# Kernel tuning notes

Hardware: AMD Instinct MI355X
Metric: run time of the kernel (lower is better)

## Reference

```python
import jax, jax.numpy as jnp
import numpy as np

T, B, D_IN = 128, 256, 600   # timesteps, batch, encoded input dim
N_RIMS, K_ACT = 6, 4          # rims per layer, active rims (top-k)
D_HID = 600 // N_RIMS         # hidden dim per RIM = 100
D_K, D_V = 64, 400            # input-attention key/value proj dims (in_d_v = cell input dim)


def setup_inputs() -> dict:
    key = jax.random.key(0)
    ks = jax.random.split(key, 8)
    g = lambda k, shape, s: (jax.random.normal(k, shape, jnp.float32) * s)
    return {
        "x": jax.random.normal(ks[0], (T, B, D_IN), jnp.float32),
        # input attention: per-RIM query proj, shared key/value proj over encoded input
        "Wq": g(ks[1], (N_RIMS, D_HID, D_K), 0.05),
        "Wk": g(ks[2], (D_IN, D_K), 0.05),
        "Wv": g(ks[3], (D_IN, D_V), 0.05),
        # block-diagonal (per-RIM) GRU params
        "W_ih": g(ks[4], (N_RIMS, D_V, 3 * D_HID), 0.05),
        "W_hh": g(ks[5], (N_RIMS, D_HID, 3 * D_HID), 0.05),
        "b_ih": jnp.zeros((N_RIMS, 3 * D_HID), jnp.float32),
        "b_hh": jnp.zeros((N_RIMS, 3 * D_HID), jnp.float32),
    }


def reference(x, Wq, Wk, Wv, W_ih, W_hh, b_ih, b_hh):
    scale = 1.0 / jnp.sqrt(jnp.float32(D_K))

    def step(h, xt):
        # --- input attention over [real input, null row] (num_modules_read_input = 2) ---
        kx = xt @ Wk                                   # [B, D_K] key for real input (null key = 0)
        vx = xt @ Wv                                   # [B, D_V] value for real input (null value = 0)
        q = jnp.einsum('bnh,nhk->bnk', h, Wq)          # [B, N, D_K] per-RIM queries
        s_in = jnp.einsum('bnk,bk->bn', q, kx) * scale # score vs real input; null score = 0
        probs = jax.nn.softmax(jnp.stack([s_in, jnp.zeros_like(s_in)], axis=-1), axis=-1)
        p_in = probs[..., 0]                           # [B, N] attention on real input
        attn_out = p_in[..., None] * vx[:, None, :]    # [B, N, D_V] (null value is zero)
        # --- active-RIM mask: top-k rims attending most to the real input ---
        _, idx = jax.lax.top_k(p_in, K_ACT)            # [B, K]
        mask = jnp.zeros_like(p_in).at[jnp.arange(B)[:, None], idx].set(1.0)[..., None]  # [B, N, 1]
        # --- block-diagonal GRU cell (blockified params: independent per RIM) ---
        gi = jnp.einsum('bnd,ndk->bnk', attn_out, W_ih) + b_ih
        gh = jnp.einsum('bnh,nhk->bnk', h, W_hh) + b_hh
        i_r, i_z, i_n = jnp.split(gi, 3, axis=-1)
        h_r, h_z, h_n = jnp.split(gh, 3, axis=-1)
        r = jax.nn.sigmoid(i_r + h_r)
        z = jax.nn.sigmoid(i_z + h_z)
        n = jnp.tanh(i_n + r * h_n)
        h_new = (1.0 - z) * n + z * h
        # inactive rims keep their old state; output is mask * hidden
        h_next = mask * h_new + (1.0 - mask) * h
        return h_next, mask * h_new                    # [B, N, D_HID]

    h0 = jnp.zeros((B, N_RIMS, D_HID), x.dtype)
    _, out = jax.lax.scan(step, h0, x)                 # out: [T, B, N_RIMS, D_HID]
    return out
```

## Files before the change

### kernel.cpp

```cpp
#include <hip/hip_runtime.h>
#include <cstddef>

#define TSTEPS 128
#define BATCH  256
#define DIN    600
#define NR     6
#define KACT   4
#define DH     100
#define DK     64
#define DV     400
#define G3     300
#define LD1    512
#define LDG    1920

__global__ __launch_bounds__(256) void build_w1(const float* __restrict__ Wk,
                                                const float* __restrict__ Wv,
                                                float* __restrict__ W1) {
  int idx = blockIdx.x * 256 + threadIdx.x;
  if (idx >= DIN * LD1) return;
  int d = idx >> 9, c = idx & (LD1 - 1);
  float v = 0.f;
  if (c < DK)            v = Wk[d * DK + c];
  else if (c < DK + DV)  v = Wv[d * DV + (c - DK)];
  W1[idx] = v;
}

__global__ __launch_bounds__(256) void build_wt(const float* __restrict__ Wih,
                                                float* __restrict__ WT) {
  int idx = blockIdx.x * 256 + threadIdx.x;
  if (idx >= DV * LDG) return;
  int v = idx / LDG, c = idx - v * LDG;
  float w = 0.f;
  if (c < NR * G3) { int n = c / G3, j = c - n * G3; w = Wih[(n * DV + v) * G3 + j]; }
  WT[idx] = w;
}

__global__ __launch_bounds__(256) void sgemm_k(const float* __restrict__ A, int lda,
                                               const float* __restrict__ B, int ldb,
                                               float* __restrict__ C, int ldc, int K) {
  __shared__ float As[8][132];
  __shared__ float Bs[8][128];
  const int tid = threadIdx.x;
  const int tx = tid & 15, ty = tid >> 4;
  const size_t m0 = (size_t)blockIdx.x * 128, n0 = (size_t)blockIdx.y * 128;
  const int arow = tid >> 1, akq = (tid & 1) * 4;
  const int brow = tid >> 5, bcol = (tid & 31) * 4;
  const float* Ap = A + (m0 + arow) * (size_t)lda + akq;
  const float* Bp = B + (size_t)brow * ldb + n0 + bcol;

  float acc[8][8];
#pragma unroll
  for (int i = 0; i < 8; ++i)
#pragma unroll
    for (int j = 0; j < 8; ++j) acc[i][j] = 0.f;

  for (int k0 = 0; k0 < K; k0 += 8) {
    float4 av = *(const float4*)(Ap + k0);
    float4 bv = *(const float4*)(Bp + (size_t)k0 * ldb);
    __syncthreads();
    As[akq + 0][arow] = av.x;
    As[akq + 1][arow] = av.y;
    As[akq + 2][arow] = av.z;
    As[akq + 3][arow] = av.w;
    *(float4*)&Bs[brow][bcol] = bv;
    __syncthreads();
#pragma unroll
    for (int k = 0; k < 8; ++k) {
      float a[8], b[8];
#pragma unroll
      for (int i = 0; i < 8; ++i) a[i] = As[k][ty * 8 + i];
#pragma unroll
      for (int j = 0; j < 8; ++j) b[j] = Bs[k][tx * 8 + j];
#pragma unroll
      for (int i = 0; i < 8; ++i)
#pragma unroll
        for (int j = 0; j < 8; ++j) acc[i][j] += a[i] * b[j];
    }
  }

  float* Cp = C + (m0 + (size_t)ty * 8) * ldc + n0 + tx * 8;
#pragma unroll
  for (int i = 0; i < 8; ++i) {
    float4 v0 = make_float4(acc[i][0], acc[i][1], acc[i][2], acc[i][3]);
    float4 v1 = make_float4(acc[i][4], acc[i][5], acc[i][6], acc[i][7]);
    *(float4*)(Cp + (size_t)i * ldc)     = v0;
    *(float4*)(Cp + (size_t)i * ldc + 4) = v1;
  }
}

__global__ __launch_bounds__(512) void rim_scan(
    const float* __restrict__ PRE1, const float* __restrict__ GX,
    const float* __restrict__ Wq,   const float* __restrict__ Whh,
    const float* __restrict__ bih,  const float* __restrict__ bhh,
    float* __restrict__ out, float* __restrict__ hstate,
    unsigned long long* __restrict__ pbuf,
    int t0, int tc, int first) {
  __shared__ __align__(16) float wbuf[G3 * DH];
  __shared__ __align__(16) float wqbuf[DK * DH];
  __shared__ __align__(16) float hbuf[8 * DH];
  __shared__ float pl[8][NR];

  const int tid = threadIdx.x;
  const int g = blockIdx.x & 31;
  const int n = blockIdx.x >> 5;

  {
    const float* wsrc = Whh + (size_t)n * (DH * G3);
    for (int i = tid; i < DH * G3; i += 512) {
      int hh = i / G3, c = i - hh * G3;
      wbuf[c * DH + hh] = wsrc[i];
    }
    const float* qsrc = Wq + (size_t)n * (DH * DK);
    for (int i = tid; i < DH * DK; i += 512) {
      int hh = i >> 6, k = i & 63;
      wqbuf[k * DH + hh] = qsrc[i];
    }
    if (first) {
      for (int i = tid; i < 8 * DH; i += 512) hbuf[i] = 0.f;
    } else {
      for (int i = tid; i < 8 * DH; i += 512) {
        int b = i / DH, hh = i - b * DH;
        hbuf[b * DH + hh] = hstate[((size_t)(g * 8 + b) * NR + n) * DH + hh];
      }
    }
  }
  __syncthreads();

  const bool isQ = tid >= 256;
  const int ho = tid & 127;
  const bool act_t = (!isQ) && (ho < DH);
  const int half = (tid >> 7) & 1;
  const int bbase = half * 4;
  const int kq = tid & 63;
  const int bp2 = (tid >> 6) & 3;

  float bi0 = 0.f, bi1 = 0.f, bi2 = 0.f, bh0 = 0.f, bh1 = 0.f, bh2 = 0.f;
  if (act_t) {
    const float* bi = bih + (size_t)n * G3 + ho;
    const float* bh = bhh + (size_t)n * G3 + ho;
    bi0 = bi[0]; bi1 = bi[DH]; bi2 = bi[2 * DH];
    bh0 = bh[0]; bh1 = bh[DH]; bh2 = bh[2 * DH];
  }

  const float4* wr = (const float4*)&wbuf[ho * DH];
  const float4* wz = (const float4*)&wbuf[(ho + 100) * DH];
  const float4* wn = (const float4*)&wbuf[(ho + 200) * DH];
  const float4* wq4 = (const float4*)&wqbuf[kq * DH];
  const float4* h40 = (const float4*)&hbuf[(bbase + 0) * DH];
  const float4* h41 = (const float4*)&hbuf[(bbase + 1) * DH];
  const float4* h42 = (const float4*)&hbuf[(bbase + 2) * DH];
  const float4* h43 = (const float4*)&hbuf[(bbase + 3) * DH];
  const float4* hqA = (const float4*)&hbuf[bp2 * DH];
  const float4* hqB = (const float4*)&hbuf[(bp2 + 4) * DH];

  for (int tl = 0; tl < tc; ++tl) {
    const int t = t0 + tl;
    const int par = t & 1;

    float gx[4][3];
    float acc[4][3];

    if (isQ) {
      float kx0 = PRE1[((size_t)tl * BATCH + g * 8 + bp2) * LD1 + kq];
      float kx1 = PRE1[((size_t)tl * BATCH + g * 8 + bp2 + 4) * LD1 + kq];
      float a0 = 0.f, a1 = 0.f;
#pragma unroll 5
      for (int q4 = 0; q4 < 25; ++q4) {
        float4 w = wq4[q4];
        float4 v0 = hqA[q4];
        float4 v1 = hqB[q4];
        a0 += v0.x * w.x; a0 += v0.y * w.y; a0 += v0.z * w.z; a0 += v0.w * w.w;
        a1 += v1.x * w.x; a1 += v1.y * w.y; a1 += v1.z * w.z; a1 += v1.w * w.w;
      }
      float s0 = a0 * kx0, s1 = a1 * kx1;
#pragma unroll
      for (int off = 1; off < 64; off <<= 1) {
        s0 += __shfl_xor(s0, off);
        s1 += __shfl_xor(s1, off);
      }
      if (kq == 0) {
        float sa = s0 * 0.125f;
        float ma = sa > 0.f ? sa : 0.f;
        float pa = expf(sa - ma) / (expf(sa - ma) + expf(-ma));
        float sb = s1 * 0.125f;
        float mb = sb > 0.f ? sb : 0.f;
        float pb = expf(sb - mb) / (expf(sb - mb) + expf(-mb));
        unsigned long long tag = ((unsigned long long)(unsigned)(t + 1)) << 32;
        __hip_atomic_store(&pbuf[(((size_t)par * 32 + g) * NR + n) * 8 + bp2],
                           tag | __float_as_uint(pa),
                           __ATOMIC_RELAXED, __HIP_MEMORY_SCOPE_AGENT);
        __hip_atomic_store(&pbuf[(((size_t)par * 32 + g) * NR + n) * 8 + bp2 + 4],
                           tag | __float_as_uint(pb),
                           __ATOMIC_RELAXED, __HIP_MEMORY_SCOPE_AGENT);
      }
    } else if (act_t) {
#pragma unroll
      for (int b = 0; b < 4; ++b) {
        const float* gr = GX + ((size_t)tl * BATCH + g * 8 + bbase + b) * LDG + n * G3;
        gx[b][0] = gr[ho]; gx[b][1] = gr[ho + DH]; gx[b][2] = gr[ho + 2 * DH];
      }
#pragma unroll
      for (int b = 0; b < 4; ++b) { acc[b][0] = 0.f; acc[b][1] = 0.f; acc[b][2] = 0.f; }
#pragma unroll 5
      for (int q4 = 0; q4 < 25; ++q4) {
        float4 w0 = wr[q4], w1 = wz[q4], w2 = wn[q4];
        float4 v0 = h40[q4], v1 = h41[q4], v2 = h42[q4], v3 = h43[q4];
        acc[0][0] += v0.x*w0.x; acc[0][0] += v0.y*w0.y; acc[0][0] += v0.z*w0.z; acc[0][0] += v0.w*w0.w;
        acc[0][1] += v0.x*w1.x; acc[0][1] += v0.y*w1.y; acc[0][1] += v0.z*w1.z; acc[0][1] += v0.w*w1.w;
        acc[0][2] += v0.x*w2.x; acc[0][2] += v0.y*w2.y; acc[0][2] += v0.z*w2.z; acc[0][2] += v0.w*w2.w;
        acc[1][0] += v1.x*w0.x; acc[1][0] += v1.y*w0.y; acc[1][0] += v1.z*w0.z; acc[1][0] += v1.w*w0.w;
        acc[1][1] += v1.x*w1.x; acc[1][1] += v1.y*w1.y; acc[1][1] += v1.z*w1.z; acc[1][1] += v1.w*w1.w;
        acc[1][2] += v1.x*w2.x; acc[1][2] += v1.y*w2.y; acc[1][2] += v1.z*w2.z; acc[1][2] += v1.w*w2.w;
        acc[2][0] += v2.x*w0.x; acc[2][0] += v2.y*w0.y; acc[2][0] += v2.z*w0.z; acc[2][0] += v2.w*w0.w;
        acc[2][1] += v2.x*w1.x; acc[2][1] += v2.y*w1.y; acc[2][1] += v2.z*w1.z; acc[2][1] += v2.w*w1.w;
        acc[2][2] += v2.x*w2.x; acc[2][2] += v2.y*w2.y; acc[2][2] += v2.z*w2.z; acc[2][2] += v2.w*w2.w;
        acc[3][0] += v3.x*w0.x; acc[3][0] += v3.y*w0.y; acc[3][0] += v3.z*w0.z; acc[3][0] += v3.w*w0.w;
        acc[3][1] += v3.x*w1.x; acc[3][1] += v3.y*w1.y; acc[3][1] += v3.z*w1.z; acc[3][1] += v3.w*w1.w;
        acc[3][2] += v3.x*w2.x; acc[3][2] += v3.y*w2.y; acc[3][2] += v3.z*w2.z; acc[3][2] += v3.w*w2.w;
      }
    }

    if (tid < 48) {
      int b = tid & 7, r = tid >> 3;
      const unsigned want = (unsigned)(t + 1);
      unsigned long long v;
      for (;;) {
        v = __hip_atomic_load(&pbuf[(((size_t)par * 32 + g) * NR + r) * 8 + b],
                              __ATOMIC_RELAXED, __HIP_MEMORY_SCOPE_AGENT);
        if ((unsigned)(v >> 32) == want) break;
        __builtin_amdgcn_s_sleep(1);
      }
      pl[b][r] = __uint_as_float((unsigned)v);
    }
    __syncthreads();

    if (act_t) {
#pragma unroll
      for (int b = 0; b < 4; ++b) {
        const int bb = bbase + b;
        float p = pl[bb][n];
        int c = 0;
#pragma unroll
        for (int r = 0; r < NR; ++r) {
          float q = pl[bb][r];
          if (q > p || (q == p && r < n)) ++c;
        }
        float m = (c < KACT) ? 1.f : 0.f;
        float grv = acc[b][0] + bh0;
        float gzv = acc[b][1] + bh1;
        float gnv = acc[b][2] + bh2;
        float ir  = p * gx[b][0] + bi0;
        float iz  = p * gx[b][1] + bi1;
        float inn = p * gx[b][2] + bi2;
        float rr = 1.f / (1.f + expf(-(ir + grv)));
        float zz = 1.f / (1.f + expf(-(iz + gzv)));
        float nn = tanhf(inn + rr * gnv);
        float hprev = hbuf[bb * DH + ho];
        float hnew = (1.f - zz) * nn + zz * hprev;
        out[(((size_t)t * BATCH + g * 8 + bb) * NR + n) * DH + ho] = m * hnew;
        hbuf[bb * DH + ho] = (m > 0.f) ? hnew : hprev;
      }
    }
    __syncthreads();
  }

  for (int i = tid; i < 8 * DH; i += 512) {
    int b = i / DH, hh = i - b * DH;
    hstate[((size_t)(g * 8 + b) * NR + n) * DH + hh] = hbuf[b * DH + hh];
  }
}

extern "C" void kernel_launch(void* const* d_in, const int* in_sizes, int n_in,
                              void* d_out, int out_size, void* d_ws, size_t ws_size,
                              hipStream_t stream) {
  const float* x   = (const float*)d_in[0];
  const float* Wq  = (const float*)d_in[1];
  const float* Wk  = (const float*)d_in[2];
  const float* Wv  = (const float*)d_in[3];
  const float* Wih = (const float*)d_in[4];
  const float* Whh = (const float*)d_in[5];
  const float* bih = (const float*)d_in[6];
  const float* bhh = (const float*)d_in[7];
  float* out = (float*)d_out;
  char* ws = (char*)d_ws;

  const size_t W1_BYTES   = (size_t)DIN * LD1 * 4;
  const size_t WT_BYTES   = (size_t)DV * LDG * 4;
  const size_t H_BYTES    = (size_t)BATCH * 600 * 4;
  const size_t PBUF_BYTES = 2 * 32 * NR * 8 * 8;
  const size_t FIXED = W1_BYTES + WT_BYTES + H_BYTES + PBUF_BYTES;
  const size_t PER_STEP = (size_t)BATCH * (LD1 + LDG) * 4;

  float* W1     = (float*)ws;
  float* WT     = (float*)(ws + W1_BYTES);
  float* hstate = (float*)(ws + W1_BYTES + WT_BYTES);
  unsigned long long* pbuf =
      (unsigned long long*)(ws + W1_BYTES + WT_BYTES + H_BYTES);

  long long avail = (long long)ws_size - (long long)FIXED;
  int TC = 1;
  if (avail > 0) {
    long long t = avail / (long long)PER_STEP;
    TC = (int)(t < 1 ? 1 : (t > TSTEPS ? TSTEPS : t));
  }
  float* PRE1 = (float*)(ws + FIXED);
  float* GXb  = (float*)(ws + FIXED + (size_t)TC * BATCH * LD1 * 4);

  build_w1<<<(DIN * LD1) / 256, 256, 0, stream>>>(Wk, Wv, W1);
  build_wt<<<(DV * LDG) / 256, 256, 0, stream>>>(Wih, WT);

  for (int t0 = 0; t0 < TSTEPS; ) {
    int tc = TSTEPS - t0 < TC ? TSTEPS - t0 : TC;
    dim3 g1(tc * 2, LD1 / 128);
    sgemm_k<<<g1, 256, 0, stream>>>(x + (size_t)t0 * BATCH * DIN, DIN, W1, LD1, PRE1, LD1, DIN);
    dim3 g2(tc * 2, LDG / 128);
    sgemm_k<<<g2, 256, 0, stream>>>(PRE1 + DK, LD1, WT, LDG, GXb, LDG, DV);
    rim_scan<<<32 * NR, 512, 0, stream>>>(PRE1, GXb, Wq, Whh, bih, bhh, out, hstate,
                                          pbuf, t0, tc, t0 == 0 ? 1 : 0);
    t0 += tc;
  }
}
```

Baseline: 1.957 ms.

## Enlarge SGEMM tile to 256x128 with double-buffered padded shared memory

```diff
diff --git a/kernel.cpp b/kernel.cpp
--- a/kernel.cpp
+++ b/kernel.cpp
@@ -12,6 +12,7 @@
 #define G3     300
 #define LD1    512
 #define LDG    1920
+#define KB     8
 
 __global__ __launch_bounds__(256) void build_w1(const float* __restrict__ Wk,
                                                 const float* __restrict__ Wv,
@@ -38,49 +39,73 @@
 __global__ __launch_bounds__(256) void sgemm_k(const float* __restrict__ A, int lda,
                                                const float* __restrict__ B, int ldb,
                                                float* __restrict__ C, int ldc, int K) {
-  __shared__ float As[8][132];
-  __shared__ float Bs[8][128];
+  __shared__ float As[2][KB][320];
+  __shared__ float Bs[2][KB][192];
   const int tid = threadIdx.x;
-  const int tx = tid & 15, ty = tid >> 4;
-  const size_t m0 = (size_t)blockIdx.x * 128, n0 = (size_t)blockIdx.y * 128;
-  const int arow = tid >> 1, akq = (tid & 1) * 4;
+  const int tx = tid & 15;
+  const int ty = tid >> 4;
+  const size_t m0 = (size_t)blockIdx.x * 256, n0 = (size_t)blockIdx.y * 128;
+
+  const float* Ap = A + (m0 + tid) * (size_t)lda;
   const int brow = tid >> 5, bcol = (tid & 31) * 4;
-  const float* Ap = A + (m0 + arow) * (size_t)lda + akq;
   const float* Bp = B + (size_t)brow * ldb + n0 + bcol;
-
-  float acc[8][8];
-#pragma unroll
-  for (int i = 0; i < 8; ++i)
+  const int aphys = tid + ((tid >> 4) << 2);
+  const int bphys = bcol + ((bcol >> 3) << 2);
+
+  float acc[16][8];
+#pragma unroll
+  for (int i = 0; i < 16; ++i)
 #pragma unroll
     for (int j = 0; j < 8; ++j) acc[i][j] = 0.f;
 
-  for (int k0 = 0; k0 < K; k0 += 8) {
-    float4 av = *(const float4*)(Ap + k0);
-    float4 bv = *(const float4*)(Bp + (size_t)k0 * ldb);
-    __syncthreads();
-    As[akq + 0][arow] = av.x;
-    As[akq + 1][arow] = av.y;
-    As[akq + 2][arow] = av.z;
-    As[akq + 3][arow] = av.w;
-    *(float4*)&Bs[brow][bcol] = bv;
-    __syncthreads();
-#pragma unroll
-    for (int k = 0; k < 8; ++k) {
-      float a[8], b[8];
-#pragma unroll
-      for (int i = 0; i < 8; ++i) a[i] = As[k][ty * 8 + i];
-#pragma unroll
-      for (int j = 0; j < 8; ++j) b[j] = Bs[k][tx * 8 + j];
-#pragma unroll
-      for (int i = 0; i < 8; ++i)
+  const int NT = K / KB;
+  float4 a0 = *(const float4*)(Ap);
+  float4 a1 = *(const float4*)(Ap + 4);
+  float4 b0 = *(const float4*)(Bp);
+  As[0][0][aphys] = a0.x; As[0][1][aphys] = a0.y;
+  As[0][2][aphys] = a0.z; As[0][3][aphys] = a0.w;
+  As[0][4][aphys] = a1.x; As[0][5][aphys] = a1.y;
+  As[0][6][aphys] = a1.z; As[0][7][aphys] = a1.w;
+  *(float4*)&Bs[0][brow][bphys] = b0;
+  __syncthreads();
+
+  int cur = 0;
+  for (int it = 0; it < NT; ++it) {
+    if (it + 1 < NT) {
+      const float* Ap2 = Ap + (it + 1) * KB;
+      a0 = *(const float4*)(Ap2);
+      a1 = *(const float4*)(Ap2 + 4);
+      b0 = *(const float4*)(Bp + (size_t)(it + 1) * KB * ldb);
+    }
+#pragma unroll
+    for (int k = 0; k < KB; ++k) {
+      float a[16], b[8];
+      *(float4*)&a[0]  = *(const float4*)&As[cur][k][ty * 20];
+      *(float4*)&a[4]  = *(const float4*)&As[cur][k][ty * 20 + 4];
+      *(float4*)&a[8]  = *(const float4*)&As[cur][k][ty * 20 + 8];
+      *(float4*)&a[12] = *(const float4*)&As[cur][k][ty * 20 + 12];
+      *(float4*)&b[0]  = *(const float4*)&Bs[cur][k][tx * 12];
+      *(float4*)&b[4]  = *(const float4*)&Bs[cur][k][tx * 12 + 4];
+#pragma unroll
+      for (int i = 0; i < 16; ++i)
 #pragma unroll
         for (int j = 0; j < 8; ++j) acc[i][j] += a[i] * b[j];
     }
-  }
-
-  float* Cp = C + (m0 + (size_t)ty * 8) * ldc + n0 + tx * 8;
-#pragma unroll
-  for (int i = 0; i < 8; ++i) {
+    if (it + 1 < NT) {
+      const int nxt = cur ^ 1;
+      As[nxt][0][aphys] = a0.x; As[nxt][1][aphys] = a0.y;
+      As[nxt][2][aphys] = a0.z; As[nxt][3][aphys] = a0.w;
+      As[nxt][4][aphys] = a1.x; As[nxt][5][aphys] = a1.y;
+      As[nxt][6][aphys] = a1.z; As[nxt][7][aphys] = a1.w;
+      *(float4*)&Bs[nxt][brow][bphys] = b0;
+      __syncthreads();
+      cur = nxt;
+    }
+  }
+
+  float* Cp = C + (m0 + (size_t)ty * 16) * ldc + n0 + tx * 8;
+#pragma unroll
+  for (int i = 0; i < 16; ++i) {
     float4 v0 = make_float4(acc[i][0], acc[i][1], acc[i][2], acc[i][3]);
     float4 v1 = make_float4(acc[i][4], acc[i][5], acc[i][6], acc[i][7]);
     *(float4*)(Cp + (size_t)i * ldc)     = v0;
@@ -311,9 +336,9 @@
 
   for (int t0 = 0; t0 < TSTEPS; ) {
     int tc = TSTEPS - t0 < TC ? TSTEPS - t0 : TC;
-    dim3 g1(tc * 2, LD1 / 128);
+    dim3 g1(tc, LD1 / 128);
     sgemm_k<<<g1, 256, 0, stream>>>(x + (size_t)t0 * BATCH * DIN, DIN, W1, LD1, PRE1, LD1, DIN);
-    dim3 g2(tc * 2, LDG / 128);
+    dim3 g2(tc, LDG / 128);
     sgemm_k<<<g2, 256, 0, stream>>>(PRE1 + DK, LD1, WT, LDG, GXb, LDG, DV);
     rim_scan<<<32 * NR, 512, 0, stream>>>(PRE1, GXb, Wq, Whh, bih, bhh, out, hstate,
                                           pbuf, t0, tc, t0 == 0 ? 1 : 0);
```

Result: slower. 2.530 ms (+29.3%).
